# Optimization experiments

Hardware: AMD Instinct MI355X
Metric: run time of the kernel (lower is better)

## Reference

```python
import jax, jax.numpy as jnp
import numpy as np

T = 4096
D_MODEL = 1024
H = 16          # n_heads
HD = 64         # head_dim = d_model // n_heads
LW = 64         # local_window
LT = 16         # latent_tokens
CHUNK = 32      # remote_chunk_size


def setup_inputs() -> dict:
    key = jax.random.key(0)
    ks = jax.random.split(key, 11)
    s = 0.02
    return {
        "x":  jax.random.normal(ks[0], (T, D_MODEL), dtype=jnp.float32),
        "Wq": jax.random.normal(ks[1], (D_MODEL, D_MODEL), dtype=jnp.float32) * s,
        "bq": jnp.zeros((D_MODEL,), dtype=jnp.float32),
        "Wk": jax.random.normal(ks[2], (D_MODEL, D_MODEL), dtype=jnp.float32) * s,
        "bk": jnp.zeros((D_MODEL,), dtype=jnp.float32),
        "Wv": jax.random.normal(ks[3], (D_MODEL, D_MODEL), dtype=jnp.float32) * s,
        "bv": jnp.zeros((D_MODEL,), dtype=jnp.float32),
        "Wo": jax.random.normal(ks[4], (D_MODEL, D_MODEL), dtype=jnp.float32) * s,
        "bo": jnp.zeros((D_MODEL,), dtype=jnp.float32),
        "Wg": jax.random.normal(ks[5], (H, D_MODEL), dtype=jnp.float32) * s,
        "bg": jnp.zeros((H,), dtype=jnp.float32),
    }


def reference(x, Wq, bq, Wk, bk, Wv, bv, Wo, bo, Wg, bg):
    """Runs prefill: forward_step for each token, returning per-step outputs [T, D_MODEL].

    Local cache = circular FIFO of size LW (append + pop-oldest == ring overwrite;
    softmax is permutation-invariant so slot order is irrelevant).
    Evicted tokens accumulate in pending sums; every CHUNK evictions the mean k/v
    is written into the remote latent ring of size LT (oldest overwritten).
    Attention happens BEFORE appending the current token's k/v, matching the torch code.
    """
    scale = 1.0 / np.sqrt(HD)
    Tn = x.shape[0]
    Q = (x @ Wq.T + bq).reshape(Tn, H, HD)
    K = (x @ Wk.T + bk).reshape(Tn, H, HD)
    V = (x @ Wv.T + bv).reshape(Tn, H, HD)
    G = jax.nn.sigmoid(x @ Wg.T + bg)  # [T, H] simple gate

    z = lambda *s: jnp.zeros(s, dtype=x.dtype)
    init = (z(LW, H, HD), z(LW, H, HD),   # local k/v ring
            z(LT, H, HD), z(LT, H, HD),   # remote k/v ring
            z(H, HD), z(H, HD),           # pending k/v sums
            jnp.int32(0), jnp.int32(0))   # pending count, remote count

    def step(carry, inp):
        lk, lv, rk, rv, pks, pvs, pc, rc = carry
        q, k, v, g, t = inp
        # ---- local attention over filled slots (count = min(t, LW)) ----
        lvalid = jnp.arange(LW) < jnp.minimum(t, LW)
        ls = jnp.einsum('hd,nhd->hn', q, lk) * scale
        ls = jnp.where(lvalid[None, :], ls, -1e30)
        lo = jnp.einsum('hn,nhd->hd', jax.nn.softmax(ls, axis=-1), lv)
        lo = lo * (t > 0)
        # ---- remote (compressed latent) attention ----
        rvalid = jnp.arange(LT) < jnp.minimum(rc, LT)
        rs = jnp.einsum('hd,nhd->hn', q, rk) * scale
        rs = jnp.where(rvalid[None, :], rs, -1e30)
        ro = jnp.einsum('hn,nhd->hd', jax.nn.softmax(rs, axis=-1), rv)
        ro = ro * (rc > 0)
        # ---- gate and combine ----
        gate = g[:, None]
        out = gate * lo + (1.0 - gate) * ro  # [H, HD]
        # ---- append k/v: ring write evicts token t-LW into pending ----
        pos = jnp.mod(t, LW)
        evict = (t >= LW)
        pks = pks + jnp.where(evict, lk[pos], 0.0)
        pvs = pvs + jnp.where(evict, lv[pos], 0.0)
        pc = pc + evict.astype(jnp.int32)
        lk = lk.at[pos].set(k)
        lv = lv.at[pos].set(v)
        # ---- compress pending into remote ring when CHUNK reached ----
        comp = (pc == CHUNK)
        ridx = jnp.mod(rc, LT)
        rk = jnp.where(comp, rk.at[ridx].set(pks / CHUNK), rk)
        rv = jnp.where(comp, rv.at[ridx].set(pvs / CHUNK), rv)
        rc = rc + comp.astype(jnp.int32)
        pks = jnp.where(comp, 0.0, pks)
        pvs = jnp.where(comp, 0.0, pvs)
        pc = jnp.where(comp, 0, pc)
        return (lk, lv, rk, rv, pks, pvs, pc, rc), out

    ts = jnp.arange(Tn, dtype=jnp.int32)
    _, outs = jax.lax.scan(step, init, (Q, K, V, G, ts))
    return outs.reshape(Tn, D_MODEL) @ Wo.T + bo
```

## Files before the change

### kernel.cpp

```cpp
#include <hip/hip_runtime.h>
#include <hip/hip_bf16.h>
#include <math.h>

typedef __attribute__((ext_vector_type(8))) short short8;
typedef __attribute__((ext_vector_type(4))) float f32x4;

#define TT 4096
#define DM 1024
#define NH 16
#define HD 64
#define PSTR 168

typedef __attribute__((address_space(3))) unsigned int lds_u32;
typedef __attribute__((address_space(1))) unsigned int glb_u32;

__device__ __forceinline__ void async_cp16(const void* g, void* l) {
    __builtin_amdgcn_global_load_lds((glb_u32*)g, (lds_u32*)l, 16, 0, 0);
}

__global__ __launch_bounds__(256) void cast_all(
    const float* __restrict__ x,  const float* __restrict__ wq,
    const float* __restrict__ wk, const float* __restrict__ wv,
    const float* __restrict__ wo,
    __hip_bfloat16* __restrict__ xb,  __hip_bfloat16* __restrict__ wqb,
    __hip_bfloat16* __restrict__ wkb, __hip_bfloat16* __restrict__ wvb,
    __hip_bfloat16* __restrict__ wob)
{
    int b = blockIdx.x;
    const float* src;
    __hip_bfloat16* dst;
    size_t base;
    if (b < 4096)      { src = x;  dst = xb;  base = (size_t)b * 1024; }
    else if (b < 5120) { src = wq; dst = wqb; base = (size_t)(b - 4096) * 1024; }
    else if (b < 6144) { src = wk; dst = wkb; base = (size_t)(b - 5120) * 1024; }
    else if (b < 7168) { src = wv; dst = wvb; base = (size_t)(b - 6144) * 1024; }
    else               { src = wo; dst = wob; base = (size_t)(b - 7168) * 1024; }
    size_t i = base + (size_t)threadIdx.x * 4;
    float4 v = *(const float4*)(src + i);
    __hip_bfloat16 h0 = (__hip_bfloat16)v.x;
    __hip_bfloat16 h1 = (__hip_bfloat16)v.y;
    __hip_bfloat16 h2 = (__hip_bfloat16)v.z;
    __hip_bfloat16 h3 = (__hip_bfloat16)v.w;
    ushort4 u;
    u.x = *(unsigned short*)&h0;
    u.y = *(unsigned short*)&h1;
    u.z = *(unsigned short*)&h2;
    u.w = *(unsigned short*)&h3;
    *(ushort4*)((unsigned short*)dst + i) = u;
}

template <typename OutT>
__global__ __launch_bounds__(256) void gemm128(
    const __hip_bfloat16* __restrict__ A,
    const __hip_bfloat16* __restrict__ B0, const __hip_bfloat16* __restrict__ B1,
    const __hip_bfloat16* __restrict__ B2,
    const float* __restrict__ c0, const float* __restrict__ c1, const float* __restrict__ c2,
    OutT* __restrict__ O0, OutT* __restrict__ O1, OutT* __restrict__ O2)
{
    const int K = DM;
    __shared__ __align__(16) unsigned short sA[128 * 32];
    __shared__ __align__(16) unsigned short sB[128 * 32];

    const int grp = blockIdx.y >> 3;
    const __hip_bfloat16* B = grp == 0 ? B0 : (grp == 1 ? B1 : B2);
    const float* bias       = grp == 0 ? c0 : (grp == 1 ? c1 : c2);
    OutT* O                 = grp == 0 ? O0 : (grp == 1 ? O1 : O2);

    const int tid  = threadIdx.x;
    const int w    = tid >> 6;
    const int lane = tid & 63;
    const int l16  = lane & 15;
    const int quad = lane >> 4;
    const int rowBase = blockIdx.x * 128;
    const int colBase = (blockIdx.y & 7) * 128;

    const int srow   = lane >> 2;
    const int sswz   = (srow & 3) ^ (srow >> 2);
    const int gchunk = (lane & 3) ^ sswz;
    const __hip_bfloat16* gA = A + (size_t)(rowBase + w * 32 + srow) * K + gchunk * 8;
    const __hip_bfloat16* gB = B + (size_t)(colBase + w * 32 + srow) * K + gchunk * 8;
    unsigned short* lA = sA + w * 32 * 32;
    unsigned short* lB = sB + w * 32 * 32;

    const int fswz = (l16 & 3) ^ (l16 >> 2);
    const int mrow = (w & 1) * 64;
    const int ncol = (w >> 1) * 64;

    f32x4 acc[4][4];
#pragma unroll
    for (int i = 0; i < 4; ++i)
#pragma unroll
        for (int j = 0; j < 4; ++j) acc[i][j] = (f32x4){0.f, 0.f, 0.f, 0.f};

    for (int k0 = 0; k0 < K; k0 += 32) {
        __syncthreads();
        async_cp16(gA + k0, lA);
        async_cp16(gA + k0 + (size_t)16 * K, lA + 16 * 32);
        async_cp16(gB + k0, lB);
        async_cp16(gB + k0 + (size_t)16 * K, lB + 16 * 32);
        __syncthreads();

        short8 af[4], bf[4];
#pragma unroll
        for (int mt = 0; mt < 4; ++mt)
            af[mt] = *(const short8*)&sA[(mrow + mt * 16 + l16) * 32 + (quad ^ fswz) * 8];
#pragma unroll
        for (int nt = 0; nt < 4; ++nt)
            bf[nt] = *(const short8*)&sB[(ncol + nt * 16 + l16) * 32 + (quad ^ fswz) * 8];
#pragma unroll
        for (int mt = 0; mt < 4; ++mt)
#pragma unroll
            for (int nt = 0; nt < 4; ++nt)
                acc[mt][nt] = __builtin_amdgcn_mfma_f32_16x16x32_bf16(af[mt], bf[nt], acc[mt][nt], 0, 0, 0);
    }

#pragma unroll
    for (int nt = 0; nt < 4; ++nt) {
        int col = colBase + ncol + nt * 16 + l16;
        float bv = bias[col];
#pragma unroll
        for (int mt = 0; mt < 4; ++mt) {
#pragma unroll
            for (int r = 0; r < 4; ++r) {
                int row = rowBase + mrow + mt * 16 + quad * 4 + r;
                O[(size_t)row * DM + col] = (OutT)(acc[mt][nt][r] + bv);
            }
        }
    }
}

__global__ __launch_bounds__(64) void g_kernel(
    const float* __restrict__ x,
    const float* __restrict__ Wg,
    const float* __restrict__ bg,
    float* __restrict__ G)
{
    const int t = blockIdx.x;
    const int lane = threadIdx.x;
    float xv[16];
#pragma unroll
    for (int i = 0; i < 16; ++i) xv[i] = x[(size_t)t * DM + i * 64 + lane];
    float zk = 0.f;
    for (int h = 0; h < NH; ++h) {
        float a = 0.f;
#pragma unroll
        for (int i = 0; i < 16; ++i) a += xv[i] * Wg[(size_t)h * DM + i * 64 + lane];
        for (int off = 32; off; off >>= 1) a += __shfl_xor(a, off);
        if (lane == h) zk = a;
    }
    if (lane < NH) {
        float z = zk + bg[lane];
        G[t * NH + lane] = 1.f / (1.f + __expf(-z));
    }
}

__global__ __launch_bounds__(256) void chunk_kernel(
    const __hip_bfloat16* __restrict__ K,
    const __hip_bfloat16* __restrict__ V,
    __hip_bfloat16* __restrict__ CK,
    __hip_bfloat16* __restrict__ CV)
{
    const int c = blockIdx.x;
    const int d = blockIdx.y * 256 + threadIdx.x;
    float ak = 0.f, av = 0.f;
    for (int i = 0; i < 32; ++i) {
        ak += (float)K[(size_t)(c * 32 + i) * DM + d];
        av += (float)V[(size_t)(c * 32 + i) * DM + d];
    }
    CK[(size_t)c * DM + d] = (__hip_bfloat16)(ak * (1.f / 32.f));
    CV[(size_t)c * DM + d] = (__hip_bfloat16)(av * (1.f / 32.f));
}

__global__ __launch_bounds__(256) void attn_mfma(
    const __hip_bfloat16* __restrict__ Q,
    const __hip_bfloat16* __restrict__ K,
    const __hip_bfloat16* __restrict__ V,
    const __hip_bfloat16* __restrict__ CK,
    const __hip_bfloat16* __restrict__ CV,
    const float* __restrict__ G,
    __hip_bfloat16* __restrict__ Aout)
{
    __shared__ alignas(16) unsigned short Pls[64 * PSTR];
    __shared__ alignas(16) unsigned short Vts[64 * PSTR];

    const int h   = blockIdx.y;
    const int t0  = blockIdx.x * 64;
    const int tid = threadIdx.x;
    const int w    = tid >> 6;
    const int lane = tid & 63;
    const int l16  = lane & 15;
    const int quad = lane >> 4;
    const float scale = 0.125f;

    const int rc0  = (t0 >= 96) ? ((t0 - 64) >> 5) : 0;
    const int cmin = rc0 > 16 ? rc0 - 16 : 0;

    const unsigned short* Vu  = (const unsigned short*)V;
    const unsigned short* CVu = (const unsigned short*)CV;

    {
        const int d = lane;
#pragma unroll
        for (int i = 0; i < 20; ++i) {
            int p = w * 20 + i;
            int j = p * 2;
            unsigned short v0, v1;
            if (j < 128) {
                int tok0 = t0 - 64 + j;
                int tok1 = tok0 + 1;
                tok0 = tok0 < 0 ? 0 : tok0;
                tok1 = tok1 < 0 ? 0 : tok1;
                v0 = Vu[(size_t)tok0 * DM + h * 64 + d];
                v1 = Vu[(size_t)tok1 * DM + h * 64 + d];
            } else {
                int n0 = j - 128;
                int c0 = cmin + n0;     if (c0 > 127) c0 = 127;
                int c1 = cmin + n0 + 1; if (c1 > 127) c1 = 127;
                v0 = CVu[(size_t)c0 * DM + h * 64 + d];
                v1 = CVu[(size_t)c1 * DM + h * 64 + d];
            }
            *(ushort2*)&Vts[d * PSTR + j] = (ushort2){v0, v1};
        }
    }

    const __hip_bfloat16* qp = Q + (size_t)(t0 + w * 16 + l16) * DM + h * 64 + quad * 8;
    short8 qf0 = *(const short8*)(qp);
    short8 qf1 = *(const short8*)(qp + 32);

    f32x4 sc[8];
#pragma unroll
    for (int jt = 0; jt < 8; ++jt) {
        int j = jt * 16 + l16;
        int tok = t0 - 64 + j;
        tok = tok < 0 ? 0 : tok;
        const __hip_bfloat16* kp = K + (size_t)tok * DM + h * 64 + quad * 8;
        short8 b0 = *(const short8*)(kp);
        short8 b1 = *(const short8*)(kp + 32);
        f32x4 a = __builtin_amdgcn_mfma_f32_16x16x32_bf16(qf0, b0, (f32x4){0.f,0.f,0.f,0.f}, 0, 0, 0);
        sc[jt]  = __builtin_amdgcn_mfma_f32_16x16x32_bf16(qf1, b1, a, 0, 0, 0);
    }
    f32x4 sc2[2];
#pragma unroll
    for (int jt = 0; jt < 2; ++jt) {
        int c = cmin + jt * 16 + l16;
        if (c > 127) c = 127;
        const __hip_bfloat16* cp = CK + (size_t)c * DM + h * 64 + quad * 8;
        short8 b0 = *(const short8*)(cp);
        short8 b1 = *(const short8*)(cp + 32);
        f32x4 a = __builtin_amdgcn_mfma_f32_16x16x32_bf16(qf0, b0, (f32x4){0.f,0.f,0.f,0.f}, 0, 0, 0);
        sc2[jt] = __builtin_amdgcn_mfma_f32_16x16x32_bf16(qf1, b1, a, 0, 0, 0);
    }

    __syncthreads();

    const int rbase = w * 16 + quad * 4;
    float gl[4], g2[4];
    float mx[4], sm[4], mx2[4], sm2[4];
#pragma unroll
    for (int reg = 0; reg < 4; ++reg) {
        int rr = rbase + reg;
        int t  = t0 + rr;
        float g = G[t * NH + h];
        int rc = (t >= 96) ? ((t - 64) >> 5) : 0;
        gl[reg] = (t > 0)  ? g        : 0.f;
        g2[reg] = (rc > 0) ? (1.f - g) : 0.f;

        int jlo = rr > (64 - t0) ? rr : (64 - t0);
        int jhi = rr + 63;
        float m = -1e30f;
#pragma unroll
        for (int jt = 0; jt < 8; ++jt) {
            int j = jt * 16 + l16;
            float s = (j >= jlo && j <= jhi) ? sc[jt][reg] * scale : -1e30f;
            sc[jt][reg] = s;
            m = fmaxf(m, s);
        }
        mx[reg] = m;

        int nvis = rc < 16 ? rc : 16;
        int clo = rc - nvis, chi = rc - 1;
        float m2 = -1e30f;
#pragma unroll
        for (int jt = 0; jt < 2; ++jt) {
            int c = cmin + jt * 16 + l16;
            float s = (c >= clo && c <= chi) ? sc2[jt][reg] * scale : -1e30f;
            sc2[jt][reg] = s;
            m2 = fmaxf(m2, s);
        }
        mx2[reg] = m2;
    }
#pragma unroll
    for (int off = 1; off <= 8; off <<= 1)
#pragma unroll
        for (int reg = 0; reg < 4; ++reg) {
            mx[reg]  = fmaxf(mx[reg],  __shfl_xor(mx[reg],  off));
            mx2[reg] = fmaxf(mx2[reg], __shfl_xor(mx2[reg], off));
        }
#pragma unroll
    for (int reg = 0; reg < 4; ++reg) {
        float s = 0.f, s2 = 0.f;
#pragma unroll
        for (int jt = 0; jt < 8; ++jt) {
            float p = __expf(sc[jt][reg] - mx[reg]);
            sc[jt][reg] = p;
            s += p;
        }
#pragma unroll
        for (int jt = 0; jt < 2; ++jt) {
            float p = __expf(sc2[jt][reg] - mx2[reg]);
            sc2[jt][reg] = p;
            s2 += p;
        }
        sm[reg] = s; sm2[reg] = s2;
    }
#pragma unroll
    for (int off = 1; off <= 8; off <<= 1)
#pragma unroll
        for (int reg = 0; reg < 4; ++reg) {
            sm[reg]  += __shfl_xor(sm[reg],  off);
            sm2[reg] += __shfl_xor(sm2[reg], off);
        }

#pragma unroll
    for (int reg = 0; reg < 4; ++reg) {
        float f1 = gl[reg] / sm[reg];
        float f2 = g2[reg] / sm2[reg];
        int rowoff = (rbase + reg) * PSTR;
#pragma unroll
        for (int jt = 0; jt < 8; ++jt) {
            __hip_bfloat16 hb = (__hip_bfloat16)(sc[jt][reg] * f1);
            Pls[rowoff + jt * 16 + l16] = *(unsigned short*)&hb;
        }
#pragma unroll
        for (int jt = 0; jt < 2; ++jt) {
            __hip_bfloat16 hb = (__hip_bfloat16)(sc2[jt][reg] * f2);
            Pls[rowoff + 128 + jt * 16 + l16] = *(unsigned short*)&hb;
        }
    }
    asm volatile("s_waitcnt lgkmcnt(0)" ::: "memory");

    f32x4 o[4];
#pragma unroll
    for (int nt = 0; nt < 4; ++nt) o[nt] = (f32x4){0.f, 0.f, 0.f, 0.f};
#pragma unroll
    for (int kt = 0; kt < 5; ++kt) {
        short8 a = *(const short8*)&Pls[(w * 16 + l16) * PSTR + kt * 32 + quad * 8];
#pragma unroll
        for (int nt = 0; nt < 4; ++nt) {
            int dd = nt * 16 + l16;
            short8 b = *(const short8*)&Vts[dd * PSTR + kt * 32 + quad * 8];
            o[nt] = __builtin_amdgcn_mfma_f32_16x16x32_bf16(a, b, o[nt], 0, 0, 0);
        }
    }

#pragma unroll
    for (int nt = 0; nt < 4; ++nt) {
#pragma unroll
        for (int reg = 0; reg < 4; ++reg) {
            int row = t0 + rbase + reg;
            int col = h * 64 + nt * 16 + l16;
            Aout[(size_t)row * DM + col] = (__hip_bfloat16)(o[nt][reg]);
        }
    }
}

extern "C" void kernel_launch(void* const* d_in, const int* in_sizes, int n_in,
                              void* d_out, int out_size, void* d_ws, size_t ws_size,
                              hipStream_t stream)
{
    const float* x  = (const float*)d_in[0];
    const float* Wq = (const float*)d_in[1];
    const float* bq = (const float*)d_in[2];
    const float* Wk = (const float*)d_in[3];
    const float* bk = (const float*)d_in[4];
    const float* Wv = (const float*)d_in[5];
    const float* bv = (const float*)d_in[6];
    const float* Wo = (const float*)d_in[7];
    const float* bo = (const float*)d_in[8];
    const float* Wg = (const float*)d_in[9];
    const float* bg = (const float*)d_in[10];
    float* out = (float*)d_out;

    char* ws = (char*)d_ws;
    const size_t MB = 1024 * 1024;
    __hip_bfloat16* xb  = (__hip_bfloat16*)(ws + 0 * MB);
    __hip_bfloat16* Qb  = (__hip_bfloat16*)(ws + 8 * MB);
    __hip_bfloat16* Kb  = (__hip_bfloat16*)(ws + 16 * MB);
    __hip_bfloat16* Vb  = (__hip_bfloat16*)(ws + 24 * MB);
    __hip_bfloat16* Ab  = (__hip_bfloat16*)(ws + 32 * MB);
    __hip_bfloat16* Wqb = (__hip_bfloat16*)(ws + 40 * MB);
    __hip_bfloat16* Wkb = (__hip_bfloat16*)(ws + 42 * MB);
    __hip_bfloat16* Wvb = (__hip_bfloat16*)(ws + 44 * MB);
    __hip_bfloat16* Wob = (__hip_bfloat16*)(ws + 46 * MB);
    __hip_bfloat16* CKb = (__hip_bfloat16*)(ws + 48 * MB);
    __hip_bfloat16* CVb = (__hip_bfloat16*)(ws + 48 * MB + 256*1024);
    float* Gf           = (float*)(ws + 48 * MB + 512 * 1024);

    cast_all<<<dim3(8192), 256, 0, stream>>>(x, Wq, Wk, Wv, Wo, xb, Wqb, Wkb, Wvb, Wob);

    gemm128<__hip_bfloat16><<<dim3(32, 24), 256, 0, stream>>>(
        xb, Wqb, Wkb, Wvb, bq, bk, bv, Qb, Kb, Vb);
    g_kernel<<<dim3(TT), 64, 0, stream>>>(x, Wg, bg, Gf);
    chunk_kernel<<<dim3(128, 4), 256, 0, stream>>>(Kb, Vb, CKb, CVb);
    attn_mfma<<<dim3(64, 16), 256, 0, stream>>>(Qb, Kb, Vb, CKb, CVb, Gf, Ab);
    gemm128<float><<<dim3(32, 8), 256, 0, stream>>>(
        Ab, Wob, Wob, Wob, bo, bo, bo, out, out, out);
}
```

Baseline: 194.5 us.

## Double-buffer GEMM LDS tiles and compute gate projection with MFMA

The GEMM kernel now double-buffers its LDS tiles, prefetching the next K-slice with async global-to-LDS copies while the MFMAs run on the current slice, and needs only one barrier per iteration. The gate projection, which was an fp32 per-token reduction kernel launched with 4096 blocks, becomes a bf16 MFMA kernel over 16-token tiles, with Wg added to the cast kernel. The aim is to hide global-load latency in the GEMMs and shrink the gate cost. The trade-offs are doubled LDS per block, lower gate precision, and a reliance on the async LDS loads being complete at the barrier without an explicit vmcnt wait.

```diff
diff --git a/kernel.cpp b/kernel.cpp
--- a/kernel.cpp
+++ b/kernel.cpp
@@ -21,10 +21,10 @@
 __global__ __launch_bounds__(256) void cast_all(
     const float* __restrict__ x,  const float* __restrict__ wq,
     const float* __restrict__ wk, const float* __restrict__ wv,
-    const float* __restrict__ wo,
+    const float* __restrict__ wo, const float* __restrict__ wg,
     __hip_bfloat16* __restrict__ xb,  __hip_bfloat16* __restrict__ wqb,
     __hip_bfloat16* __restrict__ wkb, __hip_bfloat16* __restrict__ wvb,
-    __hip_bfloat16* __restrict__ wob)
+    __hip_bfloat16* __restrict__ wob, __hip_bfloat16* __restrict__ wgb)
 {
     int b = blockIdx.x;
     const float* src;
@@ -34,7 +34,8 @@
     else if (b < 5120) { src = wq; dst = wqb; base = (size_t)(b - 4096) * 1024; }
     else if (b < 6144) { src = wk; dst = wkb; base = (size_t)(b - 5120) * 1024; }
     else if (b < 7168) { src = wv; dst = wvb; base = (size_t)(b - 6144) * 1024; }
-    else               { src = wo; dst = wob; base = (size_t)(b - 7168) * 1024; }
+    else if (b < 8192) { src = wo; dst = wob; base = (size_t)(b - 7168) * 1024; }
+    else               { src = wg; dst = wgb; base = (size_t)(b - 8192) * 1024; }
     size_t i = base + (size_t)threadIdx.x * 4;
     float4 v = *(const float4*)(src + i);
     __hip_bfloat16 h0 = (__hip_bfloat16)v.x;
@@ -58,8 +59,8 @@
     OutT* __restrict__ O0, OutT* __restrict__ O1, OutT* __restrict__ O2)
 {
     const int K = DM;
-    __shared__ __align__(16) unsigned short sA[128 * 32];
-    __shared__ __align__(16) unsigned short sB[128 * 32];
+    __shared__ __align__(16) unsigned short sA[2][128 * 32];
+    __shared__ __align__(16) unsigned short sB[2][128 * 32];
 
     const int grp = blockIdx.y >> 3;
     const __hip_bfloat16* B = grp == 0 ? B0 : (grp == 1 ? B1 : B2);
@@ -79,8 +80,7 @@
     const int gchunk = (lane & 3) ^ sswz;
     const __hip_bfloat16* gA = A + (size_t)(rowBase + w * 32 + srow) * K + gchunk * 8;
     const __hip_bfloat16* gB = B + (size_t)(colBase + w * 32 + srow) * K + gchunk * 8;
-    unsigned short* lA = sA + w * 32 * 32;
-    unsigned short* lB = sB + w * 32 * 32;
+    const int loff = w * 32 * 32;
 
     const int fswz = (l16 & 3) ^ (l16 >> 2);
     const int mrow = (w & 1) * 64;
@@ -92,21 +92,29 @@
 #pragma unroll
         for (int j = 0; j < 4; ++j) acc[i][j] = (f32x4){0.f, 0.f, 0.f, 0.f};
 
+    async_cp16(gA, sA[0] + loff);
+    async_cp16(gA + (size_t)16 * K, sA[0] + loff + 16 * 32);
+    async_cp16(gB, sB[0] + loff);
+    async_cp16(gB + (size_t)16 * K, sB[0] + loff + 16 * 32);
+
     for (int k0 = 0; k0 < K; k0 += 32) {
+        const int cur = (k0 >> 5) & 1;
         __syncthreads();
-        async_cp16(gA + k0, lA);
-        async_cp16(gA + k0 + (size_t)16 * K, lA + 16 * 32);
-        async_cp16(gB + k0, lB);
-        async_cp16(gB + k0 + (size_t)16 * K, lB + 16 * 32);
-        __syncthreads();
+        if (k0 + 32 < K) {
+            const int nxt = cur ^ 1;
+            async_cp16(gA + k0 + 32, sA[nxt] + loff);
+            async_cp16(gA + k0 + 32 + (size_t)16 * K, sA[nxt] + loff + 16 * 32);
+            async_cp16(gB + k0 + 32, sB[nxt] + loff);
+            async_cp16(gB + k0 + 32 + (size_t)16 * K, sB[nxt] + loff + 16 * 32);
+        }
 
         short8 af[4], bf[4];
 #pragma unroll
         for (int mt = 0; mt < 4; ++mt)
-            af[mt] = *(const short8*)&sA[(mrow + mt * 16 + l16) * 32 + (quad ^ fswz) * 8];
+            af[mt] = *(const short8*)&sA[cur][(mrow + mt * 16 + l16) * 32 + (quad ^ fswz) * 8];
 #pragma unroll
         for (int nt = 0; nt < 4; ++nt)
-            bf[nt] = *(const short8*)&sB[(ncol + nt * 16 + l16) * 32 + (quad ^ fswz) * 8];
+            bf[nt] = *(const short8*)&sB[cur][(ncol + nt * 16 + l16) * 32 + (quad ^ fswz) * 8];
 #pragma unroll
         for (int mt = 0; mt < 4; ++mt)
 #pragma unroll
@@ -129,28 +137,31 @@
     }
 }
 
-__global__ __launch_bounds__(64) void g_kernel(
-    const float* __restrict__ x,
-    const float* __restrict__ Wg,
+__global__ __launch_bounds__(64) void g_mfma(
+    const __hip_bfloat16* __restrict__ xb,
+    const __hip_bfloat16* __restrict__ Wgb,
     const float* __restrict__ bg,
     float* __restrict__ G)
 {
-    const int t = blockIdx.x;
     const int lane = threadIdx.x;
-    float xv[16];
-#pragma unroll
-    for (int i = 0; i < 16; ++i) xv[i] = x[(size_t)t * DM + i * 64 + lane];
-    float zk = 0.f;
-    for (int h = 0; h < NH; ++h) {
-        float a = 0.f;
-#pragma unroll
-        for (int i = 0; i < 16; ++i) a += xv[i] * Wg[(size_t)h * DM + i * 64 + lane];
-        for (int off = 32; off; off >>= 1) a += __shfl_xor(a, off);
-        if (lane == h) zk = a;
-    }
-    if (lane < NH) {
-        float z = zk + bg[lane];
-        G[t * NH + lane] = 1.f / (1.f + __expf(-z));
+    const int l16  = lane & 15;
+    const int quad = lane >> 4;
+    const int t0   = blockIdx.x * 16;
+    const __hip_bfloat16* ap = xb + (size_t)(t0 + l16) * DM + quad * 8;
+    const __hip_bfloat16* bp = Wgb + (size_t)l16 * DM + quad * 8;
+    f32x4 acc = (f32x4){0.f, 0.f, 0.f, 0.f};
+#pragma unroll 4
+    for (int k0 = 0; k0 < DM; k0 += 32) {
+        short8 a = *(const short8*)(ap + k0);
+        short8 b = *(const short8*)(bp + k0);
+        acc = __builtin_amdgcn_mfma_f32_16x16x32_bf16(a, b, acc, 0, 0, 0);
+    }
+    float bgv = bg[l16];
+#pragma unroll
+    for (int r = 0; r < 4; ++r) {
+        int t = t0 + quad * 4 + r;
+        float z = acc[r] + bgv;
+        G[t * NH + l16] = 1.f / (1.f + __expf(-z));
     }
 }
 
@@ -395,12 +406,14 @@
     __hip_bfloat16* CKb = (__hip_bfloat16*)(ws + 48 * MB);
     __hip_bfloat16* CVb = (__hip_bfloat16*)(ws + 48 * MB + 256*1024);
     float* Gf           = (float*)(ws + 48 * MB + 512 * 1024);
-
-    cast_all<<<dim3(8192), 256, 0, stream>>>(x, Wq, Wk, Wv, Wo, xb, Wqb, Wkb, Wvb, Wob);
+    __hip_bfloat16* Wgb = (__hip_bfloat16*)(ws + 48 * MB + 768*1024);
+
+    cast_all<<<dim3(8208), 256, 0, stream>>>(x, Wq, Wk, Wv, Wo, Wg,
+                                             xb, Wqb, Wkb, Wvb, Wob, Wgb);
 
     gemm128<__hip_bfloat16><<<dim3(32, 24), 256, 0, stream>>>(
         xb, Wqb, Wkb, Wvb, bq, bk, bv, Qb, Kb, Vb);
-    g_kernel<<<dim3(TT), 64, 0, stream>>>(x, Wg, bg, Gf);
+    g_mfma<<<dim3(256), 64, 0, stream>>>(xb, Wgb, bg, Gf);
     chunk_kernel<<<dim3(128, 4), 256, 0, stream>>>(Kb, Vb, CKb, CVb);
     attn_mfma<<<dim3(64, 16), 256, 0, stream>>>(Qb, Kb, Vb, CKb, CVb, Gf, Ab);
     gemm128<float><<<dim3(32, 8), 256, 0, stream>>>(
```

Result: faster. 183.1 us (-5.9%).
